# Kernel tuning notes

Hardware: AMD Instinct MI355X
Metric: run time of the kernel (lower is better)

The kernel has to match this reference:

```python
import jax, jax.numpy as jnp
import numpy as np

B, N, NC = 16, 25200, 80          # batch, anchors (640px, 3 scales x 3 anchors), classes
CONF = 0.25                        # nms_conf_thres
IOU_T = 0.45                       # nms_iou_thres
MAX_DET = 300                      # nms_max_det
K = 4096                           # fixed candidate budget (yolov5 max_nms cap, static shape)
MAX_WH = 7680.0                    # class offset for class-aware NMS
NEG = -1e9


def setup_inputs() -> dict:
    key = jax.random.key(0)
    k1, k2, k3, k4 = jax.random.split(key, 4)
    xy = jax.random.uniform(k1, (B, N, 2)) * 640.0          # box centers in pixels
    wh = jax.random.uniform(k2, (B, N, 2)) * 158.0 + 2.0    # box sizes
    obj = jax.random.uniform(k3, (B, N, 1))                 # objectness (post-sigmoid)
    cls = jax.random.uniform(k4, (B, N, NC))                # class probs (post-sigmoid)
    pred = jnp.concatenate([xy, wh, obj, cls], axis=-1)     # [B, N, 85]
    return {"pred": pred}


def xywh2xyxy(x):
    xy, wh = x[..., :2], x[..., 2:4]
    return jnp.concatenate([xy - wh * 0.5, xy + wh * 0.5], axis=-1)


def _nms_single(oboxes, scores):
    """Greedy NMS on one image. oboxes [K,4] class-offset xyxy, scores [K]
    (invalid candidates already set to NEG). Returns (idx [MAX_DET], valid [MAX_DET])."""
    areas = (oboxes[:, 2] - oboxes[:, 0]) * (oboxes[:, 3] - oboxes[:, 1])

    def step(s, _):
        i = jnp.argmax(s)
        sv = s[i] > CONF                      # selection is valid
        b = oboxes[i]
        lt = jnp.maximum(b[:2], oboxes[:, :2])
        rb = jnp.minimum(b[2:], oboxes[:, 2:])
        wh = jnp.clip(rb - lt, 0.0)
        inter = wh[:, 0] * wh[:, 1]
        area_b = (b[2] - b[0]) * (b[3] - b[1])
        iou = inter / (area_b + areas - inter + 1e-7)
        supp = (iou > IOU_T) & sv
        s2 = jnp.where(supp, NEG, s).at[i].set(NEG)  # drop suppressed + self
        return s2, (i, sv)

    _, (idx, valid) = jax.lax.scan(step, scores, None, length=MAX_DET)
    return idx, valid


def reference(pred) -> jnp.ndarray:
    boxes = xywh2xyxy(pred[..., :4])                      # [B, N, 4]
    scores = pred[..., 4:5] * pred[..., 5:]               # conf = obj * cls, [B, N, NC]
    flat = scores.reshape(B, N * NC)
    flat = jnp.where(flat > CONF, flat, NEG)              # multi_label conf filter
    cand_s, cand_i = jax.lax.top_k(flat, K)               # [B, K]
    anchor = cand_i // NC
    cls_id = cand_i % NC
    cboxes = jnp.take_along_axis(boxes, anchor[..., None], axis=1)   # [B, K, 4]
    off = (cls_id.astype(pred.dtype) * MAX_WH)[..., None]
    oboxes = cboxes + off                                  # class-offset boxes

    idx, valid = jax.vmap(_nms_single)(oboxes, cand_s)     # [B, MAX_DET]

    sel_box = jnp.take_along_axis(cboxes, idx[..., None], axis=1)   # [B, MAX_DET, 4]
    sel_s = jnp.take_along_axis(cand_s, idx, axis=1)                 # [B, MAX_DET]
    sel_c = jnp.take_along_axis(cls_id, idx, axis=1).astype(pred.dtype)
    out = jnp.concatenate([sel_box, sel_s[..., None], sel_c[..., None]], axis=-1)
    out = out * valid[..., None].astype(pred.dtype)        # zero padded rows
    return out  # [B, MAX_DET, 6] = (x1,y1,x2,y2,conf,cls)
```

## Files before the change

kernel.cpp:

```cpp
#include <hip/hip_runtime.h>
#include <stdint.h>

namespace {
typedef unsigned long long u64;
constexpr int B = 16, N = 25200, NC = 80, ROW = 85;
constexpr float IOU_T = 0.45f, MAX_WH = 7680.0f;
constexpr int MAX_DET = 300, KSEL = 4096;
constexpr uint32_t BIN_BASE = 0x3E800000u;
constexpr int T1BIN = 224;
constexpr uint32_t T1BITS = BIN_BASE + ((uint32_t)T1BIN << 16);
constexpr int NHB = 32;
constexpr int NCOPY = 8;
constexpr int NBLKX = (N + 63) / 64;
constexpr int SUBCAP = 6144;
constexpr int BCAP = 320;
constexpr int PBCAP = 3072;
constexpr int SURVCAP = 4096;
constexpr int TCAP = 2048;

constexpr size_t SURV_OFF = 0;
constexpr size_t SURV_SZ  = (size_t)B * NCOPY * SURVCAP * 8;
constexpr size_t SPEC_OFF = SURV_OFF + SURV_SZ;
constexpr size_t SPEC_SZ  = (size_t)B * NCOPY * SUBCAP * 8;
constexpr size_t GBUF_OFF = SPEC_OFF + SPEC_SZ;
constexpr size_t GBUF_SZ  = (size_t)B * NC * BCAP * 8;
constexpr size_t GBC_OFF  = GBUF_OFF + GBUF_SZ;
constexpr size_t GBC_SZ   = (size_t)B * NC * 4;
constexpr size_t HIST_OFF = GBC_OFF + GBC_SZ;
constexpr size_t HIST_SZ  = (size_t)NCOPY * B * NHB * 4;
constexpr size_t SPCC_OFF = HIST_OFF + HIST_SZ;
constexpr size_t SPCC_SZ  = (size_t)B * NCOPY * 32 * 4;
constexpr size_t SCNT_OFF = SPCC_OFF + SPCC_SZ;
constexpr size_t SCNT_SZ  = (size_t)B * NCOPY * 32 * 4;
constexpr size_t FBF_OFF  = SCNT_OFF + SCNT_SZ;
constexpr size_t FBF_SZ   = (size_t)B * NC * 4;
constexpr size_t ZERO_SZ  = HIST_SZ + SPCC_SZ + SCNT_SZ + FBF_SZ;
constexpr size_t CUTK_OFF = FBF_OFF + FBF_SZ;
constexpr int ZERO_INTS = (int)(ZERO_SZ / 4);
}

#define GLD_LDS16(gsrc, ldst) __builtin_amdgcn_global_load_lds( \
    (const __attribute__((address_space(1))) uint32_t*)(gsrc),  \
    (__attribute__((address_space(3))) uint32_t*)(ldst), 16, 0, 0)

__global__ __launch_bounds__(256) void k_zero(int* __restrict__ z) {
  int i = blockIdx.x * 256 + threadIdx.x;
  if (i < ZERO_INTS) z[i] = 0;
}

__device__ __forceinline__ void compute_pivot(const int* __restrict__ hist,
                                              int img, int tid,
                                              u64& t64lo, u64& t64hi, int& nd) {
  __shared__ int gh[NHB];
  __shared__ u64 s_lo, s_hi;
  __shared__ int s_nd;
  if (tid < NHB) {
    int s = 0;
#pragma unroll
    for (int c = 0; c < NCOPY; ++c) s += hist[((size_t)c * B + img) * NHB + tid];
    gh[tid] = s;
  }
  __syncthreads();
  if (tid == 0) {
    int cum = 0, bstar = -1, need_ = 0;
    for (int hb = NHB - 1; hb >= 0; --hb) {
      int prev = cum;
      cum += gh[hb];
      if (cum >= KSEL) { bstar = hb; need_ = KSEL - prev; break; }
    }
    if (bstar < 0) { bstar = 0; need_ = 1 << 20; }
    uint32_t tb = T1BITS + ((uint32_t)bstar << 16);
    s_lo = ((u64)tb) << 32;
    s_hi = (T1BIN + bstar >= 255) ? ~0ull : ((u64)(tb + 0x10000u) << 32);
    s_nd = need_;
  }
  __syncthreads();
  t64lo = s_lo; t64hi = s_hi; nd = s_nd;
}

__global__ __launch_bounds__(256) void k_score(const float* __restrict__ pred,
                                               int* __restrict__ speccnt,
                                               u64* __restrict__ spec,
                                               int* __restrict__ hist) {
#pragma clang fp contract(off)
  __shared__ float tile[64 * ROW];
  __shared__ int lh[NHB];
  __shared__ int blkcnt, blkbase;
  if (threadIdx.x < NHB) lh[threadIdx.x] = 0;
  if (threadIdx.x == 0) blkcnt = 0;
  const int img = blockIdx.y;
  const int r0 = blockIdx.x * 64;
  const int rows = min(64, N - r0);
  const int nf4 = rows * ROW / 4;
  const float4* src = (const float4*)(pred + ((size_t)img * N + r0) * ROW);
  float4* dst = (float4*)tile;
  for (int i = threadIdx.x; i < nf4; i += 256)
    GLD_LDS16(src + i, dst + i);
  __syncthreads();
  const int row = threadIdx.x >> 2;
  const int c0 = (threadIdx.x & 3) * 20;
  uint32_t mask = 0;
  int loc = 0;
  if (row < rows) {
    const float* tr = tile + row * ROW;
    const float obj = tr[4];
    for (int j = 0; j < 20; ++j) {
      float s = obj * tr[5 + c0 + j];
      uint32_t bits = __float_as_uint(s);
      if (bits >= T1BITS && s > 0.0f) {
        atomicAdd(&lh[(bits - T1BITS) >> 16], 1);
        mask |= (1u << j);
      }
    }
    int c = __popc(mask);
    if (c) loc = atomicAdd(&blkcnt, c);
  }
  __syncthreads();
  const int part = (blockIdx.y * gridDim.x + blockIdx.x) & (NCOPY - 1);
  if (threadIdx.x == 0)
    blkbase = atomicAdd(&speccnt[(img * NCOPY + part) * 32], blkcnt);
  __syncthreads();
  if (threadIdx.x < NHB) {
    int v = lh[threadIdx.x];
    if (v) atomicAdd(&hist[((size_t)part * B + img) * NHB + threadIdx.x], v);
  }
  if (mask) {
    const float* tr = tile + row * ROW;
    const float obj = tr[4];
    int pos = blkbase + loc;
    uint32_t m = mask;
    u64* SP = spec + ((size_t)img * NCOPY + part) * SUBCAP;
    while (m) {
      int j = __builtin_ctz(m);
      m &= m - 1;
      int c = c0 + j;
      float s = obj * tr[5 + c];
      if (pos < SUBCAP) {
        uint32_t fidx = (uint32_t)(r0 + row) * NC + c;
        SP[pos] = ((u64)__float_as_uint(s) << 32) | (u64)(uint32_t)(~fidx);
      }
      pos++;
    }
  }
}

__global__ __launch_bounds__(1024) void k_filter(const u64* __restrict__ spec,
                                                 const int* __restrict__ speccnt,
                                                 const int* __restrict__ hist,
                                                 u64* __restrict__ gbuf,
                                                 int* __restrict__ gbcnt,
                                                 u64* __restrict__ cutkey) {
  __shared__ int bc[NC];
  __shared__ u64 pb[PBCAP];
  __shared__ int pc;
  __shared__ int h16[16];
  __shared__ u64 s_pH;
  __shared__ int s_nd2;
  const int img = blockIdx.x, tid = threadIdx.x;
  u64 t64lo, t64hi; int nd;
  compute_pivot(hist, img, tid, t64lo, t64hi, nd);
  if (tid < NC) bc[tid] = 0;
  if (tid == 0) pc = 0;
  __syncthreads();
  for (int part = 0; part < NCOPY; ++part) {
    const int sc_p = min(speccnt[(img * NCOPY + part) * 32], SUBCAP);
    const u64* SP = spec + ((size_t)img * NCOPY + part) * SUBCAP;
    for (int i = tid; i < sc_p; i += 1024) {
      u64 key = SP[i];
      if (key >= t64lo) {
        uint32_t c = (~(uint32_t)key) % 80u;
        int pos = atomicAdd(&bc[c], 1);
        if (pos < BCAP) gbuf[((size_t)img * NC + c) * BCAP + pos] = key;
        if (key < t64hi) {
          int p = atomicAdd(&pc, 1);
          if (p < PBCAP) pb[p] = key;
        }
      }
    }
  }
  __syncthreads();
  if (tid < NC) gbcnt[img * NC + tid] = bc[tid];
  const int P = min(pc, PBCAP);
  u64 rk[3];
#pragma unroll
  for (int j = 0; j < 3; ++j) {
    int i = tid + (j << 10);
    rk[j] = (i < P) ? (pb[i] & 0x0000FFFFFFFFFFFFull) : 0ull;
  }
  u64 pH = 0;
  int ndr = nd;
  if (nd <= P) {
    for (int r = 11; r >= 0; --r) {
      if (tid < 16) h16[tid] = 0;
      __syncthreads();
      const int sh = (r + 1) * 4;
#pragma unroll
      for (int j = 0; j < 3; ++j) {
        int i = tid + (j << 10);
        if (i < P && (rk[j] >> sh) == pH)
          atomicAdd(&h16[(rk[j] >> (r * 4)) & 15], 1);
      }
      __syncthreads();
      if (tid == 0) {
        int cum = 0, nib = 0, nd2 = ndr;
        for (int v = 15; v >= 0; --v) {
          if (cum + h16[v] >= ndr) { nib = v; nd2 = ndr - cum; break; }
          cum += h16[v];
        }
        s_pH = (pH << 4) | (u64)nib;
        s_nd2 = nd2;
      }
      __syncthreads();
      pH = s_pH;
      ndr = s_nd2;
    }
  }
  if (tid == 0) cutkey[img] = (t64lo & 0xFFFF000000000000ull) | pH;
}

__global__ __launch_bounds__(256) void k_cnms(const float* __restrict__ pred,
                                              const u64* __restrict__ gbuf,
                                              const int* __restrict__ gbcnt,
                                              const u64* __restrict__ cutkey,
                                              int* __restrict__ scnt,
                                              u64* __restrict__ surv,
                                              int* __restrict__ fbflag) {
#pragma clang fp contract(off)
  __shared__ u64 kl[256];
  __shared__ u64 sorted[256];
  __shared__ float4 boxs[256];
  __shared__ float areas[256];
  __shared__ u64 masks[256][4];
  __shared__ u64 alv[4];
  __shared__ int s_k;
  __shared__ int wsum[4], wpre[4], s_base;
  const int img = blockIdx.y, cls = blockIdx.x;
  const int tid = threadIdx.x, w = tid >> 6, lane = tid & 63;
  const int kcRaw = gbcnt[img * NC + cls];
  if (kcRaw == 0) return;
  if (kcRaw > 256) {
    if (tid == 0) fbflag[img * NC + cls] = 1;
    return;
  }
  const u64 ck = cutkey[img];
  u64 myk = 0;
  bool keep = false;
  if (tid < kcRaw) {
    myk = gbuf[((size_t)img * NC + cls) * BCAP + tid];
    keep = myk >= ck;
  }
  kl[tid] = keep ? myk : 0ull;
  __syncthreads();
  int r = 0;
  if (keep)
    for (int j = 0; j < kcRaw; ++j) r += (kl[j] > myk);
  u64 bm = __ballot(keep);
  if (lane == 0) wsum[w] = __popcll(bm);
  if (keep) sorted[r] = myk;
  __syncthreads();
  if (tid == 0) s_k = wsum[0] + wsum[1] + wsum[2] + wsum[3];
  __syncthreads();
  const int k = s_k;
  if (k == 0) return;
  if (tid < k) {
    u64 kk = sorted[tid];
    uint32_t f = ~(uint32_t)kk;
    uint32_t a = f / 80u;
    const float* p = pred + ((size_t)img * N + a) * ROW;
    float cx = p[0], cy = p[1], w_ = p[2], h_ = p[3];
    float hw = w_ * 0.5f, hh = h_ * 0.5f;
    const float off = (float)cls * MAX_WH;
    float bx = (cx - hw) + off, by = (cy - hh) + off;
    float bz = (cx + hw) + off, bw2 = (cy + hh) + off;
    boxs[tid] = make_float4(bx, by, bz, bw2);
    areas[tid] = (bz - bx) * (bw2 - by);
  }
  __syncthreads();
  if (tid < k) {
    float4 tb = boxs[tid];
    float ta = areas[tid];
    u64 m0 = 0, m1 = 0, m2 = 0, m3 = 0;
    for (int u = tid + 1; u < k; ++u) {
      float4 ub = boxs[u];
      float ua = areas[u];
      float ltx = fmaxf(tb.x, ub.x), lty = fmaxf(tb.y, ub.y);
      float rbx = fminf(tb.z, ub.z), rby = fminf(tb.w, ub.w);
      float ww = fmaxf(rbx - ltx, 0.f), hh = fmaxf(rby - lty, 0.f);
      float inter = ww * hh;
      float iou = inter / (((ta + ua) - inter) + 1e-7f);
      if (iou > IOU_T) {
        if (u < 64) m0 |= 1ull << u;
        else if (u < 128) m1 |= 1ull << (u - 64);
        else if (u < 192) m2 |= 1ull << (u - 128);
        else m3 |= 1ull << (u - 192);
      }
    }
    masks[tid][0] = m0; masks[tid][1] = m1;
    masks[tid][2] = m2; masks[tid][3] = m3;
  }
  __syncthreads();
  if (tid == 0) {
    u64 a0 = ~0ull, a1 = ~0ull, a2 = ~0ull, a3 = ~0ull;
    for (int t = 0; t < k; ++t) {
      u64 av = t < 64 ? a0 : t < 128 ? a1 : t < 192 ? a2 : a3;
      if ((av >> (t & 63)) & 1) {
        a0 &= ~masks[t][0]; a1 &= ~masks[t][1];
        a2 &= ~masks[t][2]; a3 &= ~masks[t][3];
      }
    }
    alv[0] = a0; alv[1] = a1; alv[2] = a2; alv[3] = a3;
  }
  __syncthreads();
  const int part = (img * gridDim.x + cls) & (NCOPY - 1);
  bool sv = (tid < k) && ((alv[tid >> 6] >> (tid & 63)) & 1);
  u64 sb = __ballot(sv);
  if (lane == 0) wsum[w] = __popcll(sb);
  __syncthreads();
  if (tid == 0) {
    int t0 = wsum[0], t1 = wsum[1], t2 = wsum[2], t3 = wsum[3];
    wpre[0] = 0; wpre[1] = t0; wpre[2] = t0 + t1; wpre[3] = t0 + t1 + t2;
    int tot = t0 + t1 + t2 + t3;
    s_base = tot ? atomicAdd(&scnt[(img * NCOPY + part) * 32], tot) : 0;
  }
  __syncthreads();
  if (sv) {
    int idx = s_base + wpre[w] + __popcll(sb & ((1ull << lane) - 1ull));
    if (idx < SURVCAP)
      surv[((size_t)img * NCOPY + part) * SURVCAP + idx] = sorted[tid];
  }
}

__global__ __launch_bounds__(1024) void k_rank(const float* __restrict__ pred,
                                               const u64* __restrict__ spec,
                                               const int* __restrict__ speccnt,
                                               const u64* __restrict__ cutkey,
                                               const int* __restrict__ fbflag,
                                               int* __restrict__ scnt,
                                               u64* __restrict__ surv,
                                               float* __restrict__ out) {
#pragma clang fp contract(off)
  __shared__ u64 sk[4096];
  __shared__ u64 tl[TCAP];
  __shared__ int rh[96];
  __shared__ int s_tcnt;
  __shared__ u64 s_keylo;
  __shared__ int kk;
  const int img = blockIdx.x, tid = threadIdx.x;

  int any = 0;
  for (int i = tid; i < NC; i += 1024) any |= fbflag[img * NC + i];
  if (__syncthreads_or(any)) {
    u64* keys = sk;
    uint8_t* alive = (uint8_t*)tl;
    const u64 ck = cutkey[img];
    for (int cls = 0; cls < NC; ++cls) {
      if (!fbflag[img * NC + cls]) continue;
      if (tid == 0) kk = 0;
      for (int i = tid; i < 4096; i += 1024) keys[i] = 0ull;
      __syncthreads();
      for (int part = 0; part < NCOPY; ++part) {
        const int sc_p = min(speccnt[(img * NCOPY + part) * 32], SUBCAP);
        const u64* SP = spec + ((size_t)img * NCOPY + part) * SUBCAP;
        for (int i = tid; i < sc_p; i += 1024) {
          u64 key = SP[i];
          if (key >= ck) {
            uint32_t f = ~(uint32_t)key;
            if (f % 80u == (uint32_t)cls) {
              int p = atomicAdd(&kk, 1);
              if (p < 4096) keys[p] = key;
            }
          }
        }
      }
      __syncthreads();
      const int k2 = min(kk, 4096);
      for (int size = 2; size <= 4096; size <<= 1)
        for (int stride = size >> 1; stride > 0; stride >>= 1) {
          for (int j = 0; j < 2; ++j) {
            int p = tid + (j << 10);
            int low = p & (stride - 1);
            int i1 = ((p - low) << 1) | low;
            int i2 = i1 + stride;
            u64 a = keys[i1], b = keys[i2];
            bool dsc = (i1 & size) == 0;
            if (dsc ? (a < b) : (a > b)) { keys[i1] = b; keys[i2] = a; }
          }
          __syncthreads();
        }
      for (int i = tid; i < 4096; i += 1024) alive[i] = (i < k2) ? 1 : 0;
      __syncthreads();
      const float off = (float)cls * MAX_WH;
      for (int t = 0; t < k2; ++t) {
        if (alive[t]) {
          u64 kt = keys[t];
          uint32_t f = ~(uint32_t)kt; uint32_t a_ = f / 80u;
          const float* p = pred + ((size_t)img * N + a_) * ROW;
          float cx = p[0], cy = p[1], w_ = p[2], h_ = p[3];
          float hw = w_ * 0.5f, hh = h_ * 0.5f;
          float tbx = (cx - hw) + off, tby = (cy - hh) + off;
          float tbz = (cx + hw) + off, tbw = (cy + hh) + off;
          float tba = (tbz - tbx) * (tbw - tby);
          for (int jj = t + 1 + tid; jj < k2; jj += 1024) {
            if (!alive[jj]) continue;
            u64 kj = keys[jj];
            uint32_t fj = ~(uint32_t)kj; uint32_t aj = fj / 80u;
            const float* pj = pred + ((size_t)img * N + aj) * ROW;
            float cxj = pj[0], cyj = pj[1], wj = pj[2], hj = pj[3];
            float hwj = wj * 0.5f, hhj = hj * 0.5f;
            float bx = (cxj - hwj) + off, by = (cyj - hhj) + off;
            float bz = (cxj + hwj) + off, bw2 = (cyj + hhj) + off;
            float au = (bz - bx) * (bw2 - by);
            float ltx = fmaxf(tbx, bx), lty = fmaxf(tby, by);
            float rbx = fminf(tbz, bz), rby = fminf(tbw, bw2);
            float ww = fmaxf(rbx - ltx, 0.f), hh2 = fmaxf(rby - lty, 0.f);
            float inter = ww * hh2;
            float iou = inter / (((tba + au) - inter) + 1e-7f);
            if (iou > IOU_T) alive[jj] = 0;
          }
          if (tid == 0) {
            int b2 = atomicAdd(&scnt[(img * NCOPY + 0) * 32], 1);
            if (b2 < SURVCAP)
              surv[((size_t)img * NCOPY + 0) * SURVCAP + b2] = kt;
          }
        }
        __syncthreads();
      }
      __syncthreads();
    }
  }
  __syncthreads();

  int cnts[NCOPY], offp[NCOPY];
  int S = 0;
  for (int p = 0; p < NCOPY; ++p) {
    cnts[p] = min(scnt[(img * NCOPY + p) * 32], SURVCAP);
    offp[p] = S;
    S += cnts[p];
  }
  if (S > 4096) S = 4096;
  for (int p = 0; p < NCOPY; ++p) {
    const u64* SV = surv + ((size_t)img * NCOPY + p) * SURVCAP;
    for (int i = tid; i < cnts[p]; i += 1024) {
      int d = offp[p] + i;
      if (d < 4096) sk[d] = SV[i];
    }
  }
  if (tid < 96) rh[tid] = 0;
  if (tid == 0) s_tcnt = 0;
  __syncthreads();
  const int target = min(S, MAX_DET);
  if (S > 0) {
    for (int i = tid; i < S; i += 1024) {
      uint32_t bits = (uint32_t)(sk[i] >> 32);
      uint32_t b = (bits - T1BITS) >> 16;
      if (b > 95u) b = 95u;
      atomicAdd(&rh[b], 1);
    }
    __syncthreads();
    if (tid == 0) {
      int cum = 0, cutb = 0;
      for (int b = 95; b >= 0; --b) {
        cum += rh[b];
        if (cum >= target) { cutb = b; break; }
      }
      s_keylo = ((u64)(T1BITS + ((uint32_t)cutb << 16))) << 32;
    }
    __syncthreads();
    const u64 keylo = s_keylo;
    for (int i = tid; i < S; i += 1024) {
      if (sk[i] >= keylo) {
        int p = atomicAdd(&s_tcnt, 1);
        if (p < TCAP) tl[p] = sk[i];
      }
    }
    __syncthreads();
    const int Tn = s_tcnt;
    if (Tn <= TCAP) {
      for (int t = tid; t < Tn; t += 1024) {
        const u64 mk = tl[t];
        int rank = 0;
        for (int j = 0; j < Tn; ++j) rank += (tl[j] > mk);
        if (rank < MAX_DET) {
          uint32_t f = ~(uint32_t)mk;
          uint32_t a = f / 80u;
          uint32_t c = f - a * 80u;
          const float* p = pred + ((size_t)img * N + a) * ROW;
          float cx = p[0], cy = p[1], w = p[2], h = p[3];
          float hw = w * 0.5f, hh = h * 0.5f;
          float* o = out + ((size_t)img * MAX_DET + rank) * 6;
          o[0] = cx - hw; o[1] = cy - hh; o[2] = cx + hw; o[3] = cy + hh;
          o[4] = __uint_as_float((uint32_t)(mk >> 32));
          o[5] = (float)c;
        }
      }
    } else {
      for (int r = tid; r < S; r += 1024) {
        const u64 mk = sk[r];
        int rank = 0;
        for (int j = 0; j < S; ++j) rank += (sk[j] > mk);
        if (rank < MAX_DET) {
          uint32_t f = ~(uint32_t)mk;
          uint32_t a = f / 80u;
          uint32_t c = f - a * 80u;
          const float* p = pred + ((size_t)img * N + a) * ROW;
          float cx = p[0], cy = p[1], w = p[2], h = p[3];
          float hw = w * 0.5f, hh = h * 0.5f;
          float* o = out + ((size_t)img * MAX_DET + rank) * 6;
          o[0] = cx - hw; o[1] = cy - hh; o[2] = cx + hw; o[3] = cy + hh;
          o[4] = __uint_as_float((uint32_t)(mk >> 32));
          o[5] = (float)c;
        }
      }
    }
  }
  for (int i = target + tid; i < MAX_DET; i += 1024) {
    float* o = out + ((size_t)img * MAX_DET + i) * 6;
    o[0] = 0.f; o[1] = 0.f; o[2] = 0.f; o[3] = 0.f; o[4] = 0.f; o[5] = 0.f;
  }
}

extern "C" void kernel_launch(void* const* d_in, const int* in_sizes, int n_in,
                              void* d_out, int out_size, void* d_ws, size_t ws_size,
                              hipStream_t stream) {
  const float* pred = (const float*)d_in[0];
  float* out = (float*)d_out;
  char* ws = (char*)d_ws;

  u64*   surv    = (u64*)(ws + SURV_OFF);
  u64*   spec    = (u64*)(ws + SPEC_OFF);
  u64*   gbuf    = (u64*)(ws + GBUF_OFF);
  int*   gbcnt   = (int*)(ws + GBC_OFF);
  int*   hist    = (int*)(ws + HIST_OFF);
  int*   speccnt = (int*)(ws + SPCC_OFF);
  int*   scnt    = (int*)(ws + SCNT_OFF);
  int*   fbflag  = (int*)(ws + FBF_OFF);
  u64*   cutkey  = (u64*)(ws + CUTK_OFF);

  k_zero<<<(ZERO_INTS + 255) / 256, 256, 0, stream>>>(hist);

  dim3 gbulk(NBLKX, B);
  k_score<<<gbulk, 256, 0, stream>>>(pred, speccnt, spec, hist);
  k_filter<<<B, 1024, 0, stream>>>(spec, speccnt, hist, gbuf, gbcnt, cutkey);
  dim3 gnms(NC, B);
  k_cnms<<<gnms, 256, 0, stream>>>(pred, gbuf, gbcnt, cutkey, scnt, surv, fbflag);
  k_rank<<<B, 1024, 0, stream>>>(pred, spec, speccnt, cutkey, fbflag, scnt, surv, out);
}
```

Baseline: 97.58 us.

## Replace atomic partitioned buffers with per-block segments and drop zeroing kernel

The score kernel now writes candidates, counts and histograms into a private segment per block instead of bumping global atomics on 8 shared partitions, so the separate zeroing kernel can be removed. The cut kernel reduces the per-block histograms itself and scans segments one thread per segment. Class-NMS survivors go to fixed per-class slots with plain count stores, gathered by prefix sum in the rank kernel. This trades global atomic contention and one launch for more workspace and a serial, uncoalesced per-thread scan in the cut kernel.

```diff
diff --git a/kernel.cpp b/kernel.cpp
--- a/kernel.cpp
+++ b/kernel.cpp
@@ -10,82 +10,46 @@
 constexpr int T1BIN = 224;
 constexpr uint32_t T1BITS = BIN_BASE + ((uint32_t)T1BIN << 16);
 constexpr int NHB = 32;
-constexpr int NCOPY = 8;
 constexpr int NBLKX = (N + 63) / 64;
-constexpr int SUBCAP = 6144;
+constexpr int SLOT = 5120;
 constexpr int BCAP = 320;
 constexpr int PBCAP = 3072;
-constexpr int SURVCAP = 4096;
+constexpr int SVSLOT = 256;
 constexpr int TCAP = 2048;
 
-constexpr size_t SURV_OFF = 0;
-constexpr size_t SURV_SZ  = (size_t)B * NCOPY * SURVCAP * 8;
-constexpr size_t SPEC_OFF = SURV_OFF + SURV_SZ;
-constexpr size_t SPEC_SZ  = (size_t)B * NCOPY * SUBCAP * 8;
-constexpr size_t GBUF_OFF = SPEC_OFF + SPEC_SZ;
+constexpr size_t SPEC_OFF = 0;
+constexpr size_t SPEC_SZ  = (size_t)B * NBLKX * SLOT * 8;
+constexpr size_t SPCC_OFF = SPEC_OFF + SPEC_SZ;
+constexpr size_t SPCC_SZ  = (size_t)B * NBLKX * 4;
+constexpr size_t PH_OFF   = SPCC_OFF + SPCC_SZ;
+constexpr size_t PH_SZ    = (size_t)B * NBLKX * NHB * 4;
+constexpr size_t GBUF_OFF = PH_OFF + PH_SZ;
 constexpr size_t GBUF_SZ  = (size_t)B * NC * BCAP * 8;
 constexpr size_t GBC_OFF  = GBUF_OFF + GBUF_SZ;
 constexpr size_t GBC_SZ   = (size_t)B * NC * 4;
-constexpr size_t HIST_OFF = GBC_OFF + GBC_SZ;
-constexpr size_t HIST_SZ  = (size_t)NCOPY * B * NHB * 4;
-constexpr size_t SPCC_OFF = HIST_OFF + HIST_SZ;
-constexpr size_t SPCC_SZ  = (size_t)B * NCOPY * 32 * 4;
-constexpr size_t SCNT_OFF = SPCC_OFF + SPCC_SZ;
-constexpr size_t SCNT_SZ  = (size_t)B * NCOPY * 32 * 4;
+constexpr size_t SURV_OFF = GBC_OFF + GBC_SZ;
+constexpr size_t SURV_SZ  = (size_t)B * NC * SVSLOT * 8;
+constexpr size_t SCNT_OFF = SURV_OFF + SURV_SZ;
+constexpr size_t SCNT_SZ  = (size_t)B * NC * 4;
 constexpr size_t FBF_OFF  = SCNT_OFF + SCNT_SZ;
 constexpr size_t FBF_SZ   = (size_t)B * NC * 4;
-constexpr size_t ZERO_SZ  = HIST_SZ + SPCC_SZ + SCNT_SZ + FBF_SZ;
-constexpr size_t CUTK_OFF = FBF_OFF + FBF_SZ;
-constexpr int ZERO_INTS = (int)(ZERO_SZ / 4);
+constexpr size_t FBSV_OFF = FBF_OFF + FBF_SZ;
+constexpr size_t FBSV_SZ  = (size_t)B * 4096 * 8;
+constexpr size_t CUTK_OFF = FBSV_OFF + FBSV_SZ;
 }
 
 #define GLD_LDS16(gsrc, ldst) __builtin_amdgcn_global_load_lds( \
     (const __attribute__((address_space(1))) uint32_t*)(gsrc),  \
     (__attribute__((address_space(3))) uint32_t*)(ldst), 16, 0, 0)
 
-__global__ __launch_bounds__(256) void k_zero(int* __restrict__ z) {
-  int i = blockIdx.x * 256 + threadIdx.x;
-  if (i < ZERO_INTS) z[i] = 0;
-}
-
-__device__ __forceinline__ void compute_pivot(const int* __restrict__ hist,
-                                              int img, int tid,
-                                              u64& t64lo, u64& t64hi, int& nd) {
-  __shared__ int gh[NHB];
-  __shared__ u64 s_lo, s_hi;
-  __shared__ int s_nd;
-  if (tid < NHB) {
-    int s = 0;
-#pragma unroll
-    for (int c = 0; c < NCOPY; ++c) s += hist[((size_t)c * B + img) * NHB + tid];
-    gh[tid] = s;
-  }
-  __syncthreads();
-  if (tid == 0) {
-    int cum = 0, bstar = -1, need_ = 0;
-    for (int hb = NHB - 1; hb >= 0; --hb) {
-      int prev = cum;
-      cum += gh[hb];
-      if (cum >= KSEL) { bstar = hb; need_ = KSEL - prev; break; }
-    }
-    if (bstar < 0) { bstar = 0; need_ = 1 << 20; }
-    uint32_t tb = T1BITS + ((uint32_t)bstar << 16);
-    s_lo = ((u64)tb) << 32;
-    s_hi = (T1BIN + bstar >= 255) ? ~0ull : ((u64)(tb + 0x10000u) << 32);
-    s_nd = need_;
-  }
-  __syncthreads();
-  t64lo = s_lo; t64hi = s_hi; nd = s_nd;
-}
-
 __global__ __launch_bounds__(256) void k_score(const float* __restrict__ pred,
                                                int* __restrict__ speccnt,
                                                u64* __restrict__ spec,
-                                               int* __restrict__ hist) {
+                                               int* __restrict__ phist) {
 #pragma clang fp contract(off)
   __shared__ float tile[64 * ROW];
   __shared__ int lh[NHB];
-  __shared__ int blkcnt, blkbase;
+  __shared__ int blkcnt;
   if (threadIdx.x < NHB) lh[threadIdx.x] = 0;
   if (threadIdx.x == 0) blkcnt = 0;
   const int img = blockIdx.y;
@@ -116,56 +80,74 @@
     if (c) loc = atomicAdd(&blkcnt, c);
   }
   __syncthreads();
-  const int part = (blockIdx.y * gridDim.x + blockIdx.x) & (NCOPY - 1);
-  if (threadIdx.x == 0)
-    blkbase = atomicAdd(&speccnt[(img * NCOPY + part) * 32], blkcnt);
-  __syncthreads();
-  if (threadIdx.x < NHB) {
-    int v = lh[threadIdx.x];
-    if (v) atomicAdd(&hist[((size_t)part * B + img) * NHB + threadIdx.x], v);
-  }
+  const size_t seg = (size_t)img * NBLKX + blockIdx.x;
+  if (threadIdx.x == 0) speccnt[seg] = blkcnt;
+  if (threadIdx.x < NHB) phist[seg * NHB + threadIdx.x] = lh[threadIdx.x];
   if (mask) {
     const float* tr = tile + row * ROW;
     const float obj = tr[4];
-    int pos = blkbase + loc;
+    int pos = loc;
     uint32_t m = mask;
-    u64* SP = spec + ((size_t)img * NCOPY + part) * SUBCAP;
+    u64* SP = spec + seg * SLOT;
     while (m) {
       int j = __builtin_ctz(m);
       m &= m - 1;
       int c = c0 + j;
       float s = obj * tr[5 + c];
-      if (pos < SUBCAP) {
-        uint32_t fidx = (uint32_t)(r0 + row) * NC + c;
-        SP[pos] = ((u64)__float_as_uint(s) << 32) | (u64)(uint32_t)(~fidx);
-      }
+      uint32_t fidx = (uint32_t)(r0 + row) * NC + c;
+      SP[pos] = ((u64)__float_as_uint(s) << 32) | (u64)(uint32_t)(~fidx);
       pos++;
     }
   }
 }
 
-__global__ __launch_bounds__(1024) void k_filter(const u64* __restrict__ spec,
-                                                 const int* __restrict__ speccnt,
-                                                 const int* __restrict__ hist,
-                                                 u64* __restrict__ gbuf,
-                                                 int* __restrict__ gbcnt,
-                                                 u64* __restrict__ cutkey) {
+__global__ __launch_bounds__(1024) void k_cut(const u64* __restrict__ spec,
+                                              const int* __restrict__ speccnt,
+                                              const int* __restrict__ phist,
+                                              u64* __restrict__ gbuf,
+                                              int* __restrict__ gbcnt,
+                                              u64* __restrict__ cutkey) {
+  __shared__ int gh[NHB];
   __shared__ int bc[NC];
   __shared__ u64 pb[PBCAP];
   __shared__ int pc;
   __shared__ int h16[16];
-  __shared__ u64 s_pH;
-  __shared__ int s_nd2;
+  __shared__ u64 s_pH, s_lo, s_hi;
+  __shared__ int s_nd2, s_nd;
   const int img = blockIdx.x, tid = threadIdx.x;
-  u64 t64lo, t64hi; int nd;
-  compute_pivot(hist, img, tid, t64lo, t64hi, nd);
+  if (tid < NHB) gh[tid] = 0;
   if (tid < NC) bc[tid] = 0;
   if (tid == 0) pc = 0;
   __syncthreads();
-  for (int part = 0; part < NCOPY; ++part) {
-    const int sc_p = min(speccnt[(img * NCOPY + part) * 32], SUBCAP);
-    const u64* SP = spec + ((size_t)img * NCOPY + part) * SUBCAP;
-    for (int i = tid; i < sc_p; i += 1024) {
+  {
+    const int bin = tid & 31, slice = tid >> 5;
+    int s = 0;
+    for (int blk = slice; blk < NBLKX; blk += 32)
+      s += phist[((size_t)img * NBLKX + blk) * NHB + bin];
+    if (s) atomicAdd(&gh[bin], s);
+  }
+  __syncthreads();
+  if (tid == 0) {
+    int cum = 0, bstar = -1, need_ = 0;
+    for (int hb = NHB - 1; hb >= 0; --hb) {
+      int prev = cum;
+      cum += gh[hb];
+      if (cum >= KSEL) { bstar = hb; need_ = KSEL - prev; break; }
+    }
+    if (bstar < 0) { bstar = 0; need_ = 1 << 20; }
+    uint32_t tb = T1BITS + ((uint32_t)bstar << 16);
+    s_lo = ((u64)tb) << 32;
+    s_hi = (T1BIN + bstar >= 255) ? ~0ull : ((u64)(tb + 0x10000u) << 32);
+    s_nd = need_;
+  }
+  __syncthreads();
+  const u64 t64lo = s_lo, t64hi = s_hi;
+  const int nd = s_nd;
+  if (tid < NBLKX) {
+    const size_t seg = (size_t)img * NBLKX + tid;
+    const int cnt = min(speccnt[seg], SLOT);
+    const u64* SP = spec + seg * SLOT;
+    for (int i = 0; i < cnt; ++i) {
       u64 key = SP[i];
       if (key >= t64lo) {
         uint32_t c = (~(uint32_t)key) % 80u;
@@ -233,13 +215,15 @@
   __shared__ u64 masks[256][4];
   __shared__ u64 alv[4];
   __shared__ int s_k;
-  __shared__ int wsum[4], wpre[4], s_base;
+  __shared__ int wsum[4], wpre[4];
   const int img = blockIdx.y, cls = blockIdx.x;
   const int tid = threadIdx.x, w = tid >> 6, lane = tid & 63;
   const int kcRaw = gbcnt[img * NC + cls];
-  if (kcRaw == 0) return;
-  if (kcRaw > 256) {
-    if (tid == 0) fbflag[img * NC + cls] = 1;
+  if (kcRaw == 0 || kcRaw > 256) {
+    if (tid == 0) {
+      scnt[img * NC + cls] = 0;
+      fbflag[img * NC + cls] = (kcRaw > 256) ? 1 : 0;
+    }
     return;
   }
   const u64 ck = cutkey[img];
@@ -261,7 +245,10 @@
   if (tid == 0) s_k = wsum[0] + wsum[1] + wsum[2] + wsum[3];
   __syncthreads();
   const int k = s_k;
-  if (k == 0) return;
+  if (k == 0) {
+    if (tid == 0) { scnt[img * NC + cls] = 0; fbflag[img * NC + cls] = 0; }
+    return;
+  }
   if (tid < k) {
     u64 kk = sorted[tid];
     uint32_t f = ~(uint32_t)kk;
@@ -311,7 +298,6 @@
     alv[0] = a0; alv[1] = a1; alv[2] = a2; alv[3] = a3;
   }
   __syncthreads();
-  const int part = (img * gridDim.x + cls) & (NCOPY - 1);
   bool sv = (tid < k) && ((alv[tid >> 6] >> (tid & 63)) & 1);
   u64 sb = __ballot(sv);
   if (lane == 0) wsum[w] = __popcll(sb);
@@ -319,14 +305,13 @@
   if (tid == 0) {
     int t0 = wsum[0], t1 = wsum[1], t2 = wsum[2], t3 = wsum[3];
     wpre[0] = 0; wpre[1] = t0; wpre[2] = t0 + t1; wpre[3] = t0 + t1 + t2;
-    int tot = t0 + t1 + t2 + t3;
-    s_base = tot ? atomicAdd(&scnt[(img * NCOPY + part) * 32], tot) : 0;
+    scnt[img * NC + cls] = t0 + t1 + t2 + t3;
+    fbflag[img * NC + cls] = 0;
   }
   __syncthreads();
   if (sv) {
-    int idx = s_base + wpre[w] + __popcll(sb & ((1ull << lane) - 1ull));
-    if (idx < SURVCAP)
-      surv[((size_t)img * NCOPY + part) * SURVCAP + idx] = sorted[tid];
+    int idx = wpre[w] + __popcll(sb & ((1ull << lane) - 1ull));
+    surv[((size_t)img * NC + cls) * SVSLOT + idx] = sorted[tid];
   }
 }
 
@@ -335,17 +320,19 @@
                                                const int* __restrict__ speccnt,
                                                const u64* __restrict__ cutkey,
                                                const int* __restrict__ fbflag,
-                                               int* __restrict__ scnt,
-                                               u64* __restrict__ surv,
+                                               const int* __restrict__ scnt,
+                                               const u64* __restrict__ surv,
+                                               u64* __restrict__ fbsv,
                                                float* __restrict__ out) {
 #pragma clang fp contract(off)
   __shared__ u64 sk[4096];
   __shared__ u64 tl[TCAP];
-  __shared__ int rh[96];
-  __shared__ int s_tcnt;
+  __shared__ int rh[NHB];
+  __shared__ int pf[NC + 1];
+  __shared__ int s_tcnt, s_fbn, kk;
   __shared__ u64 s_keylo;
-  __shared__ int kk;
   const int img = blockIdx.x, tid = threadIdx.x;
+  if (tid == 0) s_fbn = 0;
 
   int any = 0;
   for (int i = tid; i < NC; i += 1024) any |= fbflag[img * NC + i];
@@ -358,17 +345,15 @@
       if (tid == 0) kk = 0;
       for (int i = tid; i < 4096; i += 1024) keys[i] = 0ull;
       __syncthreads();
-      for (int part = 0; part < NCOPY; ++part) {
-        const int sc_p = min(speccnt[(img * NCOPY + part) * 32], SUBCAP);
-        const u64* SP = spec + ((size_t)img * NCOPY + part) * SUBCAP;
-        for (int i = tid; i < sc_p; i += 1024) {
+      for (int sg = 0; sg < NBLKX; ++sg) {
+        const size_t seg = (size_t)img * NBLKX + sg;
+        const int cnt = min(speccnt[seg], SLOT);
+        const u64* SP = spec + seg * SLOT;
+        for (int i = tid; i < cnt; i += 1024) {
           u64 key = SP[i];
-          if (key >= ck) {
-            uint32_t f = ~(uint32_t)key;
-            if (f % 80u == (uint32_t)cls) {
-              int p = atomicAdd(&kk, 1);
-              if (p < 4096) keys[p] = key;
-            }
+          if (key >= ck && ((~(uint32_t)key) % 80u) == (uint32_t)cls) {
+            int p = atomicAdd(&kk, 1);
+            if (p < 4096) keys[p] = key;
           }
         }
       }
@@ -418,9 +403,8 @@
             if (iou > IOU_T) alive[jj] = 0;
           }
           if (tid == 0) {
-            int b2 = atomicAdd(&scnt[(img * NCOPY + 0) * 32], 1);
-            if (b2 < SURVCAP)
-              surv[((size_t)img * NCOPY + 0) * SURVCAP + b2] = kt;
+            int b2 = s_fbn++;
+            if (b2 < 4096) fbsv[(size_t)img * 4096 + b2] = kt;
           }
         }
         __syncthreads();
@@ -430,36 +414,45 @@
   }
   __syncthreads();
 
-  int cnts[NCOPY], offp[NCOPY];
-  int S = 0;
-  for (int p = 0; p < NCOPY; ++p) {
-    cnts[p] = min(scnt[(img * NCOPY + p) * 32], SURVCAP);
-    offp[p] = S;
-    S += cnts[p];
-  }
+  if (tid < NC) pf[tid + 1] = min(scnt[img * NC + tid], SVSLOT);
+  __syncthreads();
+  if (tid == 0) {
+    pf[0] = 0;
+    for (int c = 0; c < NC; ++c) pf[c + 1] += pf[c];
+  }
+  __syncthreads();
+  int S = pf[NC];
   if (S > 4096) S = 4096;
-  for (int p = 0; p < NCOPY; ++p) {
-    const u64* SV = surv + ((size_t)img * NCOPY + p) * SURVCAP;
-    for (int i = tid; i < cnts[p]; i += 1024) {
-      int d = offp[p] + i;
-      if (d < 4096) sk[d] = SV[i];
-    }
-  }
-  if (tid < 96) rh[tid] = 0;
+  for (int idx = tid; idx < S; idx += 1024) {
+    int lo = 0, hi = NC;
+    while (hi - lo > 1) {
+      int mid = (lo + hi) >> 1;
+      if (pf[mid] <= idx) lo = mid; else hi = mid;
+    }
+    sk[idx] = surv[((size_t)img * NC + lo) * SVSLOT + (idx - pf[lo])];
+  }
+  const int fbn = s_fbn;
+  for (int i = tid; i < fbn; i += 1024) {
+    int d = S + i;
+    if (d < 4096) sk[d] = fbsv[(size_t)img * 4096 + i];
+  }
+  int S2 = S + fbn;
+  if (S2 > 4096) S2 = 4096;
+  if (tid < NHB) rh[tid] = 0;
   if (tid == 0) s_tcnt = 0;
   __syncthreads();
-  const int target = min(S, MAX_DET);
-  if (S > 0) {
-    for (int i = tid; i < S; i += 1024) {
+  const int target = min(S2, MAX_DET);
+  if (S2 > 0) {
+    for (int i = tid; i < S2; i += 1024) {
       uint32_t bits = (uint32_t)(sk[i] >> 32);
       uint32_t b = (bits - T1BITS) >> 16;
-      if (b > 95u) b = 95u;
+      if (b > (uint32_t)(NHB - 1)) b = NHB - 1;
       atomicAdd(&rh[b], 1);
     }
     __syncthreads();
     if (tid == 0) {
       int cum = 0, cutb = 0;
-      for (int b = 95; b >= 0; --b) {
+      for (int b = NHB - 1; b >= 0; --b) {
         cum += rh[b];
         if (cum >= target) { cutb = b; break; }
       }
@@ -467,7 +460,7 @@
     }
     __syncthreads();
     const u64 keylo = s_keylo;
-    for (int i = tid; i < S; i += 1024) {
+    for (int i = tid; i < S2; i += 1024) {
       if (sk[i] >= keylo) {
         int p = atomicAdd(&s_tcnt, 1);
         if (p < TCAP) tl[p] = sk[i];
@@ -494,10 +487,10 @@
         }
       }
     } else {
-      for (int r = tid; r < S; r += 1024) {
+      for (int r = tid; r < S2; r += 1024) {
         const u64 mk = sk[r];
         int rank = 0;
-        for (int j = 0; j < S; ++j) rank += (sk[j] > mk);
+        for (int j = 0; j < S2; ++j) rank += (sk[j] > mk);
         if (rank < MAX_DET) {
           uint32_t f = ~(uint32_t)mk;
           uint32_t a = f / 80u;
@@ -526,22 +519,21 @@
   float* out = (float*)d_out;
   char* ws = (char*)d_ws;
 
-  u64*   surv    = (u64*)(ws + SURV_OFF);
   u64*   spec    = (u64*)(ws + SPEC_OFF);
+  int*   speccnt = (int*)(ws + SPCC_OFF);
+  int*   phist   = (int*)(ws + PH_OFF);
   u64*   gbuf    = (u64*)(ws + GBUF_OFF);
   int*   gbcnt   = (int*)(ws + GBC_OFF);
-  int*   hist    = (int*)(ws + HIST_OFF);
-  int*   speccnt = (int*)(ws + SPCC_OFF);
+  u64*   surv    = (u64*)(ws + SURV_OFF);
   int*   scnt    = (int*)(ws + SCNT_OFF);
   int*   fbflag  = (int*)(ws + FBF_OFF);
+  u64*   fbsv    = (u64*)(ws + FBSV_OFF);
   u64*   cutkey  = (u64*)(ws + CUTK_OFF);
 
-  k_zero<<<(ZERO_INTS + 255) / 256, 256, 0, stream>>>(hist);
-
   dim3 gbulk(NBLKX, B);
-  k_score<<<gbulk, 256, 0, stream>>>(pred, speccnt, spec, hist);
-  k_filter<<<B, 1024, 0, stream>>>(spec, speccnt, hist, gbuf, gbcnt, cutkey);
+  k_score<<<gbulk, 256, 0, stream>>>(pred, speccnt, spec, phist);
+  k_cut<<<B, 1024, 0, stream>>>(spec, speccnt, phist, gbuf, gbcnt, cutkey);
   dim3 gnms(NC, B);
   k_cnms<<<gnms, 256, 0, stream>>>(pred, gbuf, gbcnt, cutkey, scnt, surv, fbflag);
-  k_rank<<<B, 1024, 0, stream>>>(pred, spec, speccnt, cutkey, fbflag, scnt, surv, out);
+  k_rank<<<B, 1024, 0, stream>>>(pred, spec, speccnt, cutkey, fbflag, scnt, surv, fbsv, out);
 }
```

Measured after the change: 113.6 us. 16.4% more time.
